# Kernel optimization log

Hardware: AMD Instinct MI355X
Metric: run time of the kernel (lower is better)

The kernel has to match this reference:

```python
import jax, jax.numpy as jnp
import numpy as np

S, D, H, G, DH = 2048, 4096, 32, 8, 128  # seq, d_in, heads, kv_groups, head_dim
GROUP = H // G


def rotate_half(x):
    x1, x2 = jnp.split(x, 2, axis=-1)
    return jnp.concatenate([-x2, x1], axis=-1)


def setup_inputs() -> dict:
    key = jax.random.key(0)
    ks = jax.random.split(key, 8)
    x = jax.random.normal(ks[0], (1, S, D), dtype=jnp.float32)
    # causal mask: True above the diagonal (positions to mask out)
    mask = jnp.triu(jnp.ones((S, S), dtype=bool), k=1)
    # standard RoPE tables
    inv_freq = 1.0 / (10000.0 ** (np.arange(0, DH, 2, dtype=np.float32) / DH))
    t = np.arange(S, dtype=np.float32)
    freqs = np.outer(t, inv_freq)                      # [S, DH/2]
    emb = np.concatenate([freqs, freqs], axis=-1)      # [S, DH]
    cos = jnp.asarray(np.cos(emb), dtype=jnp.float32)
    sin = jnp.asarray(np.sin(emb), dtype=jnp.float32)
    sc = 0.02
    Wq = jax.random.normal(ks[1], (D, H * DH), dtype=jnp.float32) * sc
    Wk = jax.random.normal(ks[2], (D, G * DH), dtype=jnp.float32) * sc
    Wv = jax.random.normal(ks[3], (D, G * DH), dtype=jnp.float32) * sc
    Wo = jax.random.normal(ks[4], (H * DH, D), dtype=jnp.float32) * sc
    return {"x": x, "mask": mask, "cos": cos, "sin": sin,
            "Wq": Wq, "Wk": Wk, "Wv": Wv, "Wo": Wo}


def reference(x, mask, cos, sin, Wq, Wk, Wv, Wo):
    xs = x[0]                                          # [S, D] (batch must be 1)
    q = (xs @ Wq).reshape(S, H, DH).transpose(1, 0, 2)   # [H, S, DH]
    k = (xs @ Wk).reshape(S, G, DH).transpose(1, 0, 2)   # [G, S, DH]
    v = (xs @ Wv).reshape(S, G, DH).transpose(1, 0, 2)   # [G, S, DH]
    # RoPE
    q = q * cos[None] + rotate_half(q) * sin[None]
    k = k * cos[None] + rotate_half(k) * sin[None]
    # GQA: repeat KV groups to match query heads
    k = jnp.repeat(k, GROUP, axis=0)                   # [H, S, DH]
    v = jnp.repeat(v, GROUP, axis=0)                   # [H, S, DH]
    scores = jnp.einsum('hsd,htd->hst', q, k)          # [H, S, S]
    scores = jnp.where(mask[None], -jnp.inf, scores)
    scores = scores / jnp.sqrt(jnp.float32(DH))
    w = jax.nn.softmax(scores, axis=-1)
    ctx = jnp.einsum('hst,htd->hsd', w, v)             # [H, S, DH]
    ctx = ctx.transpose(1, 0, 2).reshape(S, H * DH)
    out = ctx @ Wo                                     # [S, D]
    return out[None]                                   # [1, S, D]
```

## Files before the change

kernel.cpp:

```cpp
#include <hip/hip_runtime.h>
#include <hip/hip_bf16.h>
#include <cstdint>
#include <cstddef>

#define S 2048
#define D 4096
#define H 32
#define G 8
#define DH 128
#define HD (H*DH)
#define GD (G*DH)

typedef __bf16 bf16;
typedef __bf16 bf16x4 __attribute__((ext_vector_type(4)));
typedef __bf16 bf16x8 __attribute__((ext_vector_type(8)));
typedef float f32x4 __attribute__((ext_vector_type(4)));

__device__ __forceinline__ void gload16(const void* g, void* l) {
    __builtin_amdgcn_global_load_lds(
        (const __attribute__((address_space(1))) void*)g,
        (__attribute__((address_space(3))) void*)l, 16, 0, 0);
}

#define FENCE() asm volatile("" ::: "memory")
#define BARRIER() do { FENCE(); __builtin_amdgcn_s_barrier(); FENCE(); } while (0)
#define LGKM0()  do { asm volatile("s_waitcnt lgkmcnt(0)" ::: "memory"); \
                      __builtin_amdgcn_sched_barrier(0); } while (0)
#define VMCNT(n) asm volatile("s_waitcnt vmcnt(" #n ")" ::: "memory")

__global__ __launch_bounds__(256) void cast_f32_bf16(const float* __restrict__ in,
                                                     bf16* __restrict__ out, int n4)
{
    int i = blockIdx.x * 256 + threadIdx.x;
    if (i < n4) {
        float4 v = reinterpret_cast<const float4*>(in)[i];
        bf16x4 o = { (bf16)v.x, (bf16)v.y, (bf16)v.z, (bf16)v.w };
        reinterpret_cast<bf16x4*>(out)[i] = o;
    }
}

template<bool IN_F32>
__global__ __launch_bounds__(256) void transpose_to_bf16(
    const void* __restrict__ in, bf16* __restrict__ out, int R, int C)
{
    const int r0 = blockIdx.y * 64 + (threadIdx.x & 7) * 8;
    const int c0 = blockIdx.x * 256 + (threadIdx.x >> 3) * 8;
    bf16 m[8][8];
    #pragma unroll
    for (int j = 0; j < 8; ++j) {
        if constexpr (IN_F32) {
            const float* p = (const float*)in + (size_t)(r0 + j) * C + c0;
            float4 a = *reinterpret_cast<const float4*>(p);
            float4 b = *reinterpret_cast<const float4*>(p + 4);
            m[j][0] = (bf16)a.x; m[j][1] = (bf16)a.y; m[j][2] = (bf16)a.z; m[j][3] = (bf16)a.w;
            m[j][4] = (bf16)b.x; m[j][5] = (bf16)b.y; m[j][6] = (bf16)b.z; m[j][7] = (bf16)b.w;
        } else {
            const bf16* p = (const bf16*)in + (size_t)(r0 + j) * C + c0;
            bf16x8 v = *reinterpret_cast<const bf16x8*>(p);
            #pragma unroll
            for (int i = 0; i < 8; ++i) m[j][i] = v[i];
        }
    }
    #pragma unroll
    for (int i = 0; i < 8; ++i) {
        bf16x8 ov;
        #pragma unroll
        for (int j = 0; j < 8; ++j) ov[j] = m[j][i];
        *reinterpret_cast<bf16x8*>(out + (size_t)(c0 + i) * R + r0) = ov;
    }
}

__global__ __launch_bounds__(256) void rope_inplace(bf16* __restrict__ Y,
                                                    const float* __restrict__ cosT,
                                                    const float* __restrict__ sinT,
                                                    int ncols, int total, float scale)
{
    int idx = blockIdx.x * 256 + threadIdx.x;
    if (idx >= total) return;
    int pairs = ncols >> 1;
    int s = idx / pairs;
    int p = idx - s * pairs;
    int head = p >> 6;
    int d = p & 63;
    size_t base = (size_t)s * ncols + head * DH;
    float c  = cosT[s * DH + d];
    float sn = sinT[s * DH + d];
    float a = (float)Y[base + d];
    float b = (float)Y[base + d + 64];
    Y[base + d]      = (bf16)((a * c - b * sn) * scale);
    Y[base + d + 64] = (bf16)((b * c + a * sn) * scale);
}

__global__ __launch_bounds__(512) void gemm192(
    const bf16* __restrict__ A, const bf16* __restrict__ Bt,
    bf16* __restrict__ Qout, bf16* __restrict__ Kout, bf16* __restrict__ Vout, int K)
{
    extern __shared__ char smem[];
    const int tid = threadIdx.x, lane = tid & 63, wave = tid >> 6;
    const int wr = wave >> 2, wc = wave & 3;
    const int l15 = lane & 15, lhi = lane >> 4;
    const int r8 = lane >> 3, c8 = lane & 7;
    const int csw = ((c8 ^ r8) << 3);

    const int bid = blockIdx.x;
    const int swz = (bid & 7) * 32 + (bid >> 3);
    const int bm = (swz >> 5) * 256, bn = (swz & 31) * 192;
    const int NT = K >> 6;

    auto stA = [&](int buf, int u, int t) {
        gload16(A + (size_t)(bm + u * 64 + wave * 8 + r8) * K + (t << 6) + csw,
                smem + buf * 57344 + u * 8192 + wave * 1024);
    };
    auto stB = [&](int buf, int u, int t) {
        gload16(Bt + (size_t)(bn + u * 64 + wave * 8 + r8) * K + (t << 6) + csw,
                smem + buf * 57344 + 32768 + u * 8192 + wave * 1024);
    };
    auto rdA = [&](const char* Cb, int mh, int ks, bf16x8* af) {
        #pragma unroll
        for (int m = 0; m < 4; ++m) {
            int row = wr * 128 + mh * 64 + m * 16 + l15;
            int ch = (ks * 4 + lhi) ^ (l15 & 7);
            af[m] = *reinterpret_cast<const bf16x8*>(Cb + row * 128 + ch * 16);
        }
    };
    auto rdB = [&](const char* Cb, int ks, bf16x8* bfv) {
        #pragma unroll
        for (int n = 0; n < 3; ++n) {
            int row = wc * 48 + n * 16 + l15;
            int ch = (ks * 4 + lhi) ^ (l15 & 7);
            bfv[n] = *reinterpret_cast<const bf16x8*>(Cb + 32768 + row * 128 + ch * 16);
        }
    };

    f32x4 acc[8][3] = {};

    auto mm = [&](int mh, const bf16x8* af, const bf16x8* bfv) {
        LGKM0();
        __builtin_amdgcn_s_setprio(1);
        #pragma unroll
        for (int m = 0; m < 4; ++m)
            #pragma unroll
            for (int n = 0; n < 3; ++n)
                acc[mh * 4 + m][n] = __builtin_amdgcn_mfma_f32_16x16x32_bf16(
                    af[m], bfv[n], acc[mh * 4 + m][n], 0, 0, 0);
        __builtin_amdgcn_s_setprio(0);
    };

    stB(0, 0, 0); stB(0, 1, 0); stB(0, 2, 0);
    stA(0, 0, 0); stA(0, 2, 0); stA(0, 1, 0); stA(0, 3, 0);
    VMCNT(2);
    BARRIER();

    for (int t = 0; t < NT; ++t) {
        const char* Cb = smem + (t & 1) * 57344;
        const int nb = (t + 1) & 1;
        const int tn = (t + 1 < NT) ? t + 1 : t;
        bf16x8 a4[4], bk0[3], bk1[3];

        rdB(Cb, 0, bk0); rdA(Cb, 0, 0, a4);
        stB(nb, 0, tn); stB(nb, 1, tn);
        mm(0, a4, bk0);
        BARRIER();

        rdB(Cb, 1, bk1); rdA(Cb, 0, 1, a4);
        stB(nb, 2, tn); stA(nb, 0, tn);
        mm(0, a4, bk1);
        VMCNT(4);
        BARRIER();

        rdA(Cb, 1, 0, a4);
        stA(nb, 2, tn); stA(nb, 1, tn);
        mm(1, a4, bk0);
        BARRIER();

        rdA(Cb, 1, 1, a4);
        stA(nb, 3, tn);
        mm(1, a4, bk1);
        VMCNT(2);
        BARRIER();
    }

    #pragma unroll
    for (int m = 0; m < 8; ++m) {
        int r0 = bm + wr * 128 + m * 16 + lhi * 4;
        #pragma unroll
        for (int n = 0; n < 3; ++n) {
            int c = bn + wc * 48 + n * 16 + l15;
            #pragma unroll
            for (int j = 0; j < 4; ++j) {
                bf16 v = (bf16)acc[m][n][j];
                if (c < HD)            Qout[(size_t)(r0 + j) * HD + c] = v;
                else if (c < HD + GD)  Kout[(size_t)(r0 + j) * GD + (c - HD)] = v;
                else                   Vout[(size_t)(r0 + j) * GD + (c - HD - GD)] = v;
            }
        }
    }
}

__global__ __launch_bounds__(512) void gemm3b(
    const bf16* __restrict__ A, const bf16* __restrict__ Bt,
    float* __restrict__ C, int N, int K, int nbn)
{
    extern __shared__ char smem[];
    const int tid = threadIdx.x, lane = tid & 63, wave = tid >> 6;
    const int wr = wave >> 1, wc = wave & 1;
    const int l15 = lane & 15, lhi = lane >> 4;
    const int r8 = lane >> 3, c8 = lane & 7;
    const int csw = ((c8 ^ r8) << 3);

    const int nwg = gridDim.x, qq = nwg >> 3;
    const int swz = (blockIdx.x & 7) * qq + (blockIdx.x >> 3);
    const int bm = (swz / nbn) * 256, bn = (swz % nbn) * 128;
    const int NT = K >> 6;

    auto stageA = [&](int buf, int L, int t) {
        int row0 = L * 64 + wave * 8;
        gload16(A + (size_t)(bm + row0 + r8) * K + (t << 6) + csw,
                smem + buf * 49152 + row0 * 128);
    };
    auto stageB = [&](int buf, int L, int t) {
        int row0 = L * 64 + wave * 8;
        gload16(Bt + (size_t)(bn + row0 + r8) * K + (t << 6) + csw,
                smem + buf * 49152 + 32768 + row0 * 128);
    };
    auto rdA = [&](const char* Ab, int ks, bf16x8* af) {
        #pragma unroll
        for (int m = 0; m < 4; ++m) {
            int row = wr * 64 + m * 16 + l15;
            int ch = (ks * 4 + lhi) ^ (l15 & 7);
            af[m] = *reinterpret_cast<const bf16x8*>(Ab + row * 128 + ch * 16);
        }
    };
    auto rdB = [&](const char* Bb, int ks, bf16x8* bfv) {
        #pragma unroll
        for (int n = 0; n < 4; ++n) {
            int row = wc * 64 + n * 16 + l15;
            int ch = (ks * 4 + lhi) ^ (l15 & 7);
            bfv[n] = *reinterpret_cast<const bf16x8*>(Bb + row * 128 + ch * 16);
        }
    };

    f32x4 acc[4][4] = {};

    #pragma unroll
    for (int L = 0; L < 4; ++L) stageA(0, L, 0);
    stageB(0, 0, 0); stageB(0, 1, 0);
    #pragma unroll
    for (int L = 0; L < 4; ++L) stageA(1, L, 1);
    stageB(1, 0, 1); stageB(1, 1, 1);
    VMCNT(6);
    BARRIER();

    for (int t = 0; t < NT; ++t) {
        const char* Ab = smem + (t % 3) * 49152;
        const char* Bb = Ab + 32768;
        const int b2 = (t + 2) % 3;
        const int st = (t + 2 < NT) ? t + 2 : NT - 1;
        bf16x8 af[4], bk[4];

        rdB(Bb, 0, bk); rdA(Ab, 0, af);
        stageA(b2, 0, st); stageA(b2, 1, st);
        LGKM0();
        __builtin_amdgcn_s_setprio(1);
        #pragma unroll
        for (int m = 0; m < 4; ++m)
            #pragma unroll
            for (int n = 0; n < 4; ++n)
                acc[m][n] = __builtin_amdgcn_mfma_f32_16x16x32_bf16(af[m], bk[n], acc[m][n], 0, 0, 0);
        __builtin_amdgcn_s_setprio(0);

        rdB(Bb, 1, bk); rdA(Ab, 1, af);
        stageA(b2, 2, st); stageA(b2, 3, st);
        stageB(b2, 0, st); stageB(b2, 1, st);
        LGKM0();
        __builtin_amdgcn_s_setprio(1);
        #pragma unroll
        for (int m = 0; m < 4; ++m)
            #pragma unroll
            for (int n = 0; n < 4; ++n)
                acc[m][n] = __builtin_amdgcn_mfma_f32_16x16x32_bf16(af[m], bk[n], acc[m][n], 0, 0, 0);
        __builtin_amdgcn_s_setprio(0);

        VMCNT(6);
        BARRIER();
    }

    #pragma unroll
    for (int m = 0; m < 4; ++m) {
        int r0 = bm + wr * 64 + m * 16 + lhi * 4;
        #pragma unroll
        for (int n = 0; n < 4; ++n) {
            int c = bn + wc * 64 + n * 16 + l15;
            #pragma unroll
            for (int j = 0; j < 4; ++j)
                C[(size_t)(r0 + j) * N + c] = acc[m][n][j];
        }
    }
}

#define BM 128
#define BN 128
#define BK 32
#define LDSK 40

template<bool OUT_BF16>
__global__ __launch_bounds__(256) void gemm_aBf16(
    const bf16* __restrict__ A,
    const float* __restrict__ B0, const float* __restrict__ B1,
    void* __restrict__ C0, void* __restrict__ C1,
    int M, int N, int K)
{
    __shared__ alignas(16) bf16 Al[BM][LDSK];
    __shared__ alignas(16) bf16 Bt[BN][LDSK];

    const float* __restrict__ B = blockIdx.z ? B1 : B0;
    void* __restrict__ C = blockIdx.z ? C1 : C0;

    const int tid  = threadIdx.x;
    const int lane = tid & 63;
    const int wave = tid >> 6;
    const int wm = (wave >> 1) * 64;
    const int wn = (wave & 1) * 64;
    const int bm = blockIdx.y * BM;
    const int bn = blockIdx.x * BN;
    const int l15 = lane & 15;
    const int lhi = lane >> 4;

    f32x4 acc[4][4] = {};

    for (int k0 = 0; k0 < K; k0 += BK) {
        #pragma unroll
        for (int it = 0; it < 2; ++it) {
            int idx = it * 256 + tid;
            int row = idx >> 2;
            int ko  = idx & 3;
            bf16x8 v = *reinterpret_cast<const bf16x8*>(
                A + (size_t)(bm + row) * K + k0 + ko * 8);
            *reinterpret_cast<bf16x8*>(&Al[row][ko * 8]) = v;
        }
        {
            int n = tid & 127;
            int kbase = (tid >> 7) * 8;
            const float* bp = B + (size_t)k0 * N + bn + n;
            #pragma unroll
            for (int half = 0; half < 2; ++half) {
                bf16x8 v;
                #pragma unroll
                for (int j = 0; j < 8; ++j)
                    v[j] = (bf16)bp[(size_t)(half * 16 + kbase + j) * N];
                *reinterpret_cast<bf16x8*>(&Bt[n][half * 16 + kbase]) = v;
            }
        }
        __syncthreads();

        bf16x8 af[4], bfv[4];
        #pragma unroll
        for (int m = 0; m < 4; ++m)
            af[m] = *reinterpret_cast<const bf16x8*>(&Al[wm + m * 16 + l15][lhi * 8]);
        #pragma unroll
        for (int n = 0; n < 4; ++n)
            bfv[n] = *reinterpret_cast<const bf16x8*>(&Bt[wn + n * 16 + l15][lhi * 8]);
        #pragma unroll
        for (int m = 0; m < 4; ++m)
            #pragma unroll
            for (int n = 0; n < 4; ++n)
                acc[m][n] = __builtin_amdgcn_mfma_f32_16x16x32_bf16(
                    af[m], bfv[n], acc[m][n], 0, 0, 0);
        __syncthreads();
    }

    #pragma unroll
    for (int m = 0; m < 4; ++m) {
        int r0 = bm + wm + m * 16 + lhi * 4;
        #pragma unroll
        for (int n = 0; n < 4; ++n) {
            int c = bn + wn + n * 16 + l15;
            #pragma unroll
            for (int j = 0; j < 4; ++j) {
                if constexpr (OUT_BF16)
                    reinterpret_cast<bf16*>(C)[(size_t)(r0 + j) * N + c] = (bf16)acc[m][n][j];
                else
                    reinterpret_cast<float*>(C)[(size_t)(r0 + j) * N + c] = acc[m][n][j];
            }
        }
    }
}

#define QBLK 64
#define KVBLK 64
#define NQT (S/QBLK)

template<bool MASK>
__device__ __forceinline__ void attn_tile(
    int t0, int q0, int wave, int l15, int lhi,
    const bf16x8* qf, const char* Kl, const char* Vl, char* Plw,
    f32x4* o, float* m_i, float* l_i)
{
    f32x4 sc[4] = {};
    __builtin_amdgcn_s_setprio(1);
    #pragma unroll
    for (int n = 0; n < 4; ++n) {
        int row = n * 16 + l15;
        #pragma unroll
        for (int kk = 0; kk < 4; ++kk) {
            bf16x8 kf = *reinterpret_cast<const bf16x8*>(
                Kl + row * 256 + ((((kk * 4 + lhi)) ^ (l15 & 7)) << 4));
            sc[n] = __builtin_amdgcn_mfma_f32_16x16x32_bf16(qf[kk], kf, sc[n], 0, 0, 0);
        }
    }
    __builtin_amdgcn_s_setprio(0);

    float corr[4];
    #pragma unroll
    for (int j = 0; j < 4; ++j) {
        const int qr = q0 + wave * 16 + lhi * 4 + j;
        float vals[4];
        float mx = -1e30f;
        #pragma unroll
        for (int n = 0; n < 4; ++n) {
            float v = sc[n][j];
            if constexpr (MASK) {
                int t = t0 + n * 16 + l15;
                if (t > qr) v = -1e30f;
            }
            vals[n] = v;
            mx = fmaxf(mx, v);
        }
        #pragma unroll
        for (int ms = 1; ms < 16; ms <<= 1)
            mx = fmaxf(mx, __shfl_xor(mx, ms, 16));
        float mnew = fmaxf(m_i[j], mx);
        float cr = __expf(m_i[j] - mnew);
        float rsum = 0.f;
        #pragma unroll
        for (int n = 0; n < 4; ++n) {
            float p = __expf(vals[n] - mnew);
            rsum += p;
            int r = lhi * 4 + j;
            int off = ((r << 7) + ((n * 16 + l15) << 1)) ^ ((r & 7) << 4);
            *reinterpret_cast<bf16*>(Plw + off) = (bf16)p;
        }
        #pragma unroll
        for (int ms = 1; ms < 16; ms <<= 1)
            rsum += __shfl_xor(rsum, ms, 16);
        l_i[j] = l_i[j] * cr + rsum;
        m_i[j] = mnew;
        corr[j] = cr;
    }

    #pragma unroll
    for (int n = 0; n < 8; ++n)
        #pragma unroll
        for (int j = 0; j < 4; ++j)
            o[n][j] *= corr[j];

    __builtin_amdgcn_s_setprio(1);
    #pragma unroll
    for (int kk = 0; kk < 2; ++kk) {
        bf16x8 pf = *reinterpret_cast<const bf16x8*>(
            Plw + (l15 << 7) + ((((kk * 4 + lhi)) ^ (l15 & 7)) << 4));
        #pragma unroll
        for (int n = 0; n < 8; ++n) {
            int d = n * 16 + l15;
            bf16x8 vf = *reinterpret_cast<const bf16x8*>(
                Vl + (d << 7) + ((((kk * 4 + lhi)) ^ (d & 7)) << 4));
            o[n] = __builtin_amdgcn_mfma_f32_16x16x32_bf16(pf, vf, o[n], 0, 0, 0);
        }
    }
    __builtin_amdgcn_s_setprio(0);
}

__global__ __launch_bounds__(256) void flash_fwd3(
    const bf16* __restrict__ Q, const bf16* __restrict__ Kr,
    const bf16* __restrict__ VtG, bf16* __restrict__ ctx)
{
    extern __shared__ char fsm[];

    const int tid  = threadIdx.x;
    const int lane = tid & 63;
    const int wave = tid >> 6;
    const int l15 = lane & 15;
    const int lhi = lane >> 4;
    const int bid = blockIdx.x;
    const int qt = (NQT - 1) - (bid >> 5);
    const int h  = ((bid & 7) << 2) | ((bid >> 3) & 3);
    const int g  = h >> 2;
    const int q0 = qt * QBLK;
    char* Plw = fsm + 65536 + wave * 2048;

    bf16x8 qf[4];
    {
        const bf16* qp = Q + (size_t)(q0 + wave * 16 + l15) * HD + h * DH + lhi * 8;
        #pragma unroll
        for (int kk = 0; kk < 4; ++kk)
            qf[kk] = *reinterpret_cast<const bf16x8*>(qp + kk * 32);
    }

    f32x4 o[8] = {};
    float m_i[4] = { -1e30f, -1e30f, -1e30f, -1e30f };
    float l_i[4] = {};

    auto stage = [&](int t0, int buf) {
        char* Kl = fsm + buf * 32768;
        char* Vl = Kl + 16384;
        #pragma unroll
        for (int t = 0; t < 4; ++t) {
            int ch = wave * 256 + t * 64 + lane;
            {
                int row = ch >> 4, ci = ch & 15;
                gload16(Kr + (size_t)(t0 + row) * GD + g * DH + ((ci ^ (row & 7)) << 3),
                        Kl + (wave * 256 + t * 64) * 16);
            }
            {
                int d = ch >> 3, ci = ch & 7;
                gload16(VtG + (size_t)(g * DH + d) * S + t0 + ((ci ^ (d & 7)) << 3),
                        Vl + (wave * 256 + t * 64) * 16);
            }
        }
    };

    const int nt = qt + 1;
    stage(0, 0);
    VMCNT(0);
    BARRIER();

    for (int it = 0; it < nt; ++it) {
        if (it + 1 < nt) stage((it + 1) * KVBLK, (it + 1) & 1);
        const char* Kl = fsm + (it & 1) * 32768;
        const char* Vl = Kl + 16384;
        if (it == nt - 1)
            attn_tile<true>(it * KVBLK, q0, wave, l15, lhi, qf, Kl, Vl, Plw, o, m_i, l_i);
        else
            attn_tile<false>(it * KVBLK, q0, wave, l15, lhi, qf, Kl, Vl, Plw, o, m_i, l_i);
        VMCNT(0);
        BARRIER();
    }

    #pragma unroll
    for (int n = 0; n < 8; ++n) {
        int c = h * DH + n * 16 + l15;
        #pragma unroll
        for (int j = 0; j < 4; ++j) {
            int r = q0 + wave * 16 + lhi * 4 + j;
            ctx[(size_t)r * HD + c] = (bf16)(o[n][j] / l_i[j]);
        }
    }
}

extern "C" void kernel_launch(void* const* d_in, const int* in_sizes, int n_in,
                              void* d_out, int out_size, void* d_ws, size_t ws_size,
                              hipStream_t stream)
{
    const float* x    = (const float*)d_in[0];
    const float* cosT = (const float*)d_in[2];
    const float* sinT = (const float*)d_in[3];
    const float* Wq   = (const float*)d_in[4];
    const float* Wk   = (const float*)d_in[5];
    const float* Wv   = (const float*)d_in[6];
    const float* Wo   = (const float*)d_in[7];
    float* out = (float*)d_out;

    const size_t MB = (size_t)1 << 20;
    char* ws = (char*)d_ws;
    bf16* xb  = (bf16*)ws;
    bf16* ctx = (bf16*)(ws + 16 * MB);
    bf16* Qb  = (bf16*)d_out;
    bf16* Kb  = Qb + (size_t)S * HD;
    bf16* Vb  = Kb + (size_t)S * GD;
    bf16* VtG = Vb + (size_t)S * GD;

    const bool fast = ws_size >= 112 * MB;
    const float qscale = 0.08838834764831845f;

    hipFuncSetAttribute(reinterpret_cast<const void*>(&flash_fwd3),
                        hipFuncAttributeMaxDynamicSharedMemorySize, 73728);

    cast_f32_bf16<<<(S * D / 4 + 255) / 256, 256, 0, stream>>>(x, xb, S * D / 4);

    if (fast) {
        bf16* Wqkvt = (bf16*)(ws + 32 * MB);
        bf16* Wot   = (bf16*)(ws + 80 * MB);

        transpose_to_bf16<true><<<dim3(HD / 256, D / 64), 256, 0, stream>>>(Wq, Wqkvt, D, HD);
        transpose_to_bf16<true><<<dim3(GD / 256, D / 64), 256, 0, stream>>>(Wk, Wqkvt + (size_t)HD * D, D, GD);
        transpose_to_bf16<true><<<dim3(GD / 256, D / 64), 256, 0, stream>>>(Wv, Wqkvt + (size_t)(HD + GD) * D, D, GD);
        transpose_to_bf16<true><<<dim3(D / 256, HD / 64), 256, 0, stream>>>(Wo, Wot, HD, D);

        hipFuncSetAttribute(reinterpret_cast<const void*>(&gemm192),
                            hipFuncAttributeMaxDynamicSharedMemorySize, 114688);
        hipFuncSetAttribute(reinterpret_cast<const void*>(&gemm3b),
                            hipFuncAttributeMaxDynamicSharedMemorySize, 147456);

        gemm192<<<256, 512, 114688, stream>>>(xb, Wqkvt, Qb, Kb, Vb, D);

        rope_inplace<<<(S * HD / 2 + 255) / 256, 256, 0, stream>>>(Qb, cosT, sinT, HD, S * HD / 2, qscale);
        rope_inplace<<<(S * GD / 2 + 255) / 256, 256, 0, stream>>>(Kb, cosT, sinT, GD, S * GD / 2, 1.0f);

        transpose_to_bf16<false><<<dim3(GD / 256, S / 64), 256, 0, stream>>>(Vb, VtG, S, GD);

        flash_fwd3<<<NQT * H, 256, 73728, stream>>>(Qb, Kb, VtG, ctx);

        gemm3b<<<256, 512, 147456, stream>>>(ctx, Wot, out, D, HD, 32);
    } else {
        gemm_aBf16<true><<<dim3(HD / BN, S / BM, 1), 256, 0, stream>>>(
            xb, Wq, Wq, (void*)Qb, (void*)Qb, S, HD, D);
        gemm_aBf16<true><<<dim3(GD / BN, S / BM, 2), 256, 0, stream>>>(
            xb, Wk, Wv, (void*)Kb, (void*)Vb, S, GD, D);

        rope_inplace<<<(S * HD / 2 + 255) / 256, 256, 0, stream>>>(Qb, cosT, sinT, HD, S * HD / 2, qscale);
        rope_inplace<<<(S * GD / 2 + 255) / 256, 256, 0, stream>>>(Kb, cosT, sinT, GD, S * GD / 2, 1.0f);

        transpose_to_bf16<false><<<dim3(GD / 256, S / 64), 256, 0, stream>>>(Vb, VtG, S, GD);

        flash_fwd3<<<NQT * H, 256, 73728, stream>>>(Qb, Kb, VtG, ctx);

        gemm_aBf16<false><<<dim3(D / BN, S / BM, 1), 256, 0, stream>>>(
            ctx, Wo, Wo, (void*)out, (void*)out, S, D, HD);
    }

    (void)in_sizes; (void)n_in; (void)out_size; (void)ws_size;
}
```

Before: 365.4 us.

## Software-pipeline LDS reads in GEMMs and widen flash attention to 128-row Q tiles

Both projection GEMMs now prefetch the next k-slice's register fragments from LDS while MFMAs run on the current ones. Each issues a whole tile's global-to-LDS loads at once and uses partial lgkmcnt waits instead of draining to zero, which is meant to hide LDS latency behind matrix math. Flash attention moves to 512-thread blocks with 128-row query tiles and a larger shared-memory budget, so each K/V tile is reused by twice as many query rows. The costs are more register pressure, extra barriers per iteration, and fewer attention blocks. The launch_bounds occupancy hints and the changed masking logic may also affect correctness or occupancy.

```diff
diff --git a/kernel.cpp b/kernel.cpp
--- a/kernel.cpp
+++ b/kernel.cpp
@@ -24,9 +24,9 @@
 
 #define FENCE() asm volatile("" ::: "memory")
 #define BARRIER() do { FENCE(); __builtin_amdgcn_s_barrier(); FENCE(); } while (0)
-#define LGKM0()  do { asm volatile("s_waitcnt lgkmcnt(0)" ::: "memory"); \
-                      __builtin_amdgcn_sched_barrier(0); } while (0)
-#define VMCNT(n) asm volatile("s_waitcnt vmcnt(" #n ")" ::: "memory")
+#define VMCNT(n)  asm volatile("s_waitcnt vmcnt(" #n ")" ::: "memory")
+#define LGKMC(n)  do { asm volatile("s_waitcnt lgkmcnt(" #n ")" ::: "memory"); \
+                       __builtin_amdgcn_sched_barrier(0); } while (0)
 
 __global__ __launch_bounds__(256) void cast_f32_bf16(const float* __restrict__ in,
                                                      bf16* __restrict__ out, int n4)
@@ -91,7 +91,7 @@
     Y[base + d + 64] = (bf16)((b * c + a * sn) * scale);
 }
 
-__global__ __launch_bounds__(512) void gemm192(
+__global__ __launch_bounds__(512, 2) void gemm192(
     const bf16* __restrict__ A, const bf16* __restrict__ Bt,
     bf16* __restrict__ Qout, bf16* __restrict__ Kout, bf16* __restrict__ Vout, int K)
 {
@@ -107,13 +107,15 @@
     const int bm = (swz >> 5) * 256, bn = (swz & 31) * 192;
     const int NT = K >> 6;
 
-    auto stA = [&](int buf, int u, int t) {
-        gload16(A + (size_t)(bm + u * 64 + wave * 8 + r8) * K + (t << 6) + csw,
-                smem + buf * 57344 + u * 8192 + wave * 1024);
-    };
-    auto stB = [&](int buf, int u, int t) {
-        gload16(Bt + (size_t)(bn + u * 64 + wave * 8 + r8) * K + (t << 6) + csw,
-                smem + buf * 57344 + 32768 + u * 8192 + wave * 1024);
+    auto stageAll = [&](int buf, int t) {
+        #pragma unroll
+        for (int u = 0; u < 3; ++u)
+            gload16(Bt + (size_t)(bn + u * 64 + wave * 8 + r8) * K + (t << 6) + csw,
+                    smem + buf * 57344 + 32768 + u * 8192 + wave * 1024);
+        #pragma unroll
+        for (int u = 0; u < 4; ++u)
+            gload16(A + (size_t)(bm + u * 64 + wave * 8 + r8) * K + (t << 6) + csw,
+                    smem + buf * 57344 + u * 8192 + wave * 1024);
     };
     auto rdA = [&](const char* Cb, int mh, int ks, bf16x8* af) {
         #pragma unroll
@@ -133,9 +135,7 @@
     };
 
     f32x4 acc[8][3] = {};
-
-    auto mm = [&](int mh, const bf16x8* af, const bf16x8* bfv) {
-        LGKM0();
+    auto mmc = [&](int mh, const bf16x8* af, const bf16x8* bfv) {
         __builtin_amdgcn_s_setprio(1);
         #pragma unroll
         for (int m = 0; m < 4; ++m)
@@ -146,37 +146,43 @@
         __builtin_amdgcn_s_setprio(0);
     };
 
-    stB(0, 0, 0); stB(0, 1, 0); stB(0, 2, 0);
-    stA(0, 0, 0); stA(0, 2, 0); stA(0, 1, 0); stA(0, 3, 0);
-    VMCNT(2);
+    bf16x8 a_cur[4], a_nxt[4], bk0[3], bk1[3];
+
+    stageAll(0, 0);
+    VMCNT(0);
     BARRIER();
+    rdB(smem, 0, bk0);
+    rdA(smem, 0, 0, a_cur);
 
     for (int t = 0; t < NT; ++t) {
-        const char* Cb = smem + (t & 1) * 57344;
+        const char* cur = smem + (t & 1) * 57344;
+        const char* nxb = smem + ((t + 1) & 1) * 57344;
         const int nb = (t + 1) & 1;
         const int tn = (t + 1 < NT) ? t + 1 : t;
-        bf16x8 a4[4], bk0[3], bk1[3];
-
-        rdB(Cb, 0, bk0); rdA(Cb, 0, 0, a4);
-        stB(nb, 0, tn); stB(nb, 1, tn);
-        mm(0, a4, bk0);
-        BARRIER();
-
-        rdB(Cb, 1, bk1); rdA(Cb, 0, 1, a4);
-        stB(nb, 2, tn); stA(nb, 0, tn);
-        mm(0, a4, bk1);
-        VMCNT(4);
-        BARRIER();
-
-        rdA(Cb, 1, 0, a4);
-        stA(nb, 2, tn); stA(nb, 1, tn);
-        mm(1, a4, bk0);
-        BARRIER();
-
-        rdA(Cb, 1, 1, a4);
-        stA(nb, 3, tn);
-        mm(1, a4, bk1);
-        VMCNT(2);
+
+        rdA(cur, 0, 1, a_nxt);
+        rdB(cur, 1, bk1);
+        stageAll(nb, tn);
+        LGKMC(7);
+        mmc(0, a_cur, bk0);
+        BARRIER();
+
+        rdA(cur, 1, 0, a_cur);
+        LGKMC(4);
+        mmc(0, a_nxt, bk1);
+        BARRIER();
+
+        rdA(cur, 1, 1, a_nxt);
+        LGKMC(4);
+        mmc(1, a_cur, bk0);
+        BARRIER();
+
+        VMCNT(0);
+        BARRIER();
+        rdA(nxb, 0, 0, a_cur);
+        rdB(nxb, 0, bk0);
+        LGKMC(7);
+        mmc(1, a_nxt, bk1);
         BARRIER();
     }
 
@@ -197,7 +203,7 @@
     }
 }
 
-__global__ __launch_bounds__(512) void gemm3b(
+__global__ __launch_bounds__(512, 2) void gemm3b(
     const bf16* __restrict__ A, const bf16* __restrict__ Bt,
     float* __restrict__ C, int N, int K, int nbn)
 {
@@ -213,15 +219,15 @@
     const int bm = (swz / nbn) * 256, bn = (swz % nbn) * 128;
     const int NT = K >> 6;
 
-    auto stageA = [&](int buf, int L, int t) {
-        int row0 = L * 64 + wave * 8;
-        gload16(A + (size_t)(bm + row0 + r8) * K + (t << 6) + csw,
-                smem + buf * 49152 + row0 * 128);
-    };
-    auto stageB = [&](int buf, int L, int t) {
-        int row0 = L * 64 + wave * 8;
-        gload16(Bt + (size_t)(bn + row0 + r8) * K + (t << 6) + csw,
-                smem + buf * 49152 + 32768 + row0 * 128);
+    auto stageAll = [&](int buf, int t) {
+        #pragma unroll
+        for (int u = 0; u < 4; ++u)
+            gload16(A + (size_t)(bm + u * 64 + wave * 8 + r8) * K + (t << 6) + csw,
+                    smem + buf * 49152 + u * 8192 + wave * 1024);
+        #pragma unroll
+        for (int u = 0; u < 2; ++u)
+            gload16(Bt + (size_t)(bn + u * 64 + wave * 8 + r8) * K + (t << 6) + csw,
+                    smem + buf * 49152 + 32768 + u * 8192 + wave * 1024);
     };
     auto rdA = [&](const char* Ab, int ks, bf16x8* af) {
         #pragma unroll
@@ -231,57 +237,54 @@
             af[m] = *reinterpret_cast<const bf16x8*>(Ab + row * 128 + ch * 16);
         }
     };
-    auto rdB = [&](const char* Bb, int ks, bf16x8* bfv) {
+    auto rdB = [&](const char* Ab, int ks, bf16x8* bfv) {
         #pragma unroll
         for (int n = 0; n < 4; ++n) {
             int row = wc * 64 + n * 16 + l15;
             int ch = (ks * 4 + lhi) ^ (l15 & 7);
-            bfv[n] = *reinterpret_cast<const bf16x8*>(Bb + row * 128 + ch * 16);
+            bfv[n] = *reinterpret_cast<const bf16x8*>(Ab + 32768 + row * 128 + ch * 16);
         }
     };
 
     f32x4 acc[4][4] = {};
-
-    #pragma unroll
-    for (int L = 0; L < 4; ++L) stageA(0, L, 0);
-    stageB(0, 0, 0); stageB(0, 1, 0);
-    #pragma unroll
-    for (int L = 0; L < 4; ++L) stageA(1, L, 1);
-    stageB(1, 0, 1); stageB(1, 1, 1);
+    auto mmc = [&](const bf16x8* af, const bf16x8* bfv) {
+        __builtin_amdgcn_s_setprio(1);
+        #pragma unroll
+        for (int m = 0; m < 4; ++m)
+            #pragma unroll
+            for (int n = 0; n < 4; ++n)
+                acc[m][n] = __builtin_amdgcn_mfma_f32_16x16x32_bf16(af[m], bfv[n], acc[m][n], 0, 0, 0);
+        __builtin_amdgcn_s_setprio(0);
+    };
+
+    bf16x8 a_cur[4], b_cur[4], a_nxt[4], b_nxt[4];
+
+    stageAll(0, 0);
+    stageAll(1, (1 < NT) ? 1 : 0);
     VMCNT(6);
     BARRIER();
+    rdA(smem, 0, a_cur);
+    rdB(smem, 0, b_cur);
 
     for (int t = 0; t < NT; ++t) {
-        const char* Ab = smem + (t % 3) * 49152;
-        const char* Bb = Ab + 32768;
-        const int b2 = (t + 2) % 3;
+        const char* cur = smem + (t % 3) * 49152;
+        const char* nxb = smem + ((t + 1) % 3) * 49152;
+        const int sb = (t + 2) % 3;
         const int st = (t + 2 < NT) ? t + 2 : NT - 1;
-        bf16x8 af[4], bk[4];
-
-        rdB(Bb, 0, bk); rdA(Ab, 0, af);
-        stageA(b2, 0, st); stageA(b2, 1, st);
-        LGKM0();
-        __builtin_amdgcn_s_setprio(1);
-        #pragma unroll
-        for (int m = 0; m < 4; ++m)
-            #pragma unroll
-            for (int n = 0; n < 4; ++n)
-                acc[m][n] = __builtin_amdgcn_mfma_f32_16x16x32_bf16(af[m], bk[n], acc[m][n], 0, 0, 0);
-        __builtin_amdgcn_s_setprio(0);
-
-        rdB(Bb, 1, bk); rdA(Ab, 1, af);
-        stageA(b2, 2, st); stageA(b2, 3, st);
-        stageB(b2, 0, st); stageB(b2, 1, st);
-        LGKM0();
-        __builtin_amdgcn_s_setprio(1);
-        #pragma unroll
-        for (int m = 0; m < 4; ++m)
-            #pragma unroll
-            for (int n = 0; n < 4; ++n)
-                acc[m][n] = __builtin_amdgcn_mfma_f32_16x16x32_bf16(af[m], bk[n], acc[m][n], 0, 0, 0);
-        __builtin_amdgcn_s_setprio(0);
+
+        rdA(cur, 1, a_nxt);
+        rdB(cur, 1, b_nxt);
+        stageAll(sb, st);
+        LGKMC(8);
+        mmc(a_cur, b_cur);
+        BARRIER();
 
         VMCNT(6);
+        BARRIER();
+        rdA(nxb, 0, a_cur);
+        rdB(nxb, 0, b_cur);
+        LGKMC(8);
+        mmc(a_nxt, b_nxt);
         BARRIER();
     }
 
@@ -386,7 +389,7 @@
     }
 }
 
-#define QBLK 64
+#define QBLK 128
 #define KVBLK 64
 #define NQT (S/QBLK)
 
@@ -470,7 +473,7 @@
     __builtin_amdgcn_s_setprio(0);
 }
 
-__global__ __launch_bounds__(256) void flash_fwd3(
+__global__ __launch_bounds__(512, 4) void flash_fwd4(
     const bf16* __restrict__ Q, const bf16* __restrict__ Kr,
     const bf16* __restrict__ VtG, bf16* __restrict__ ctx)
 {
@@ -504,22 +507,22 @@
         char* Kl = fsm + buf * 32768;
         char* Vl = Kl + 16384;
         #pragma unroll
-        for (int t = 0; t < 4; ++t) {
-            int ch = wave * 256 + t * 64 + lane;
+        for (int t = 0; t < 2; ++t) {
+            int ch = t * 512 + tid;
             {
                 int row = ch >> 4, ci = ch & 15;
                 gload16(Kr + (size_t)(t0 + row) * GD + g * DH + ((ci ^ (row & 7)) << 3),
-                        Kl + (wave * 256 + t * 64) * 16);
+                        Kl + ch * 16);
             }
             {
                 int d = ch >> 3, ci = ch & 7;
                 gload16(VtG + (size_t)(g * DH + d) * S + t0 + ((ci ^ (d & 7)) << 3),
-                        Vl + (wave * 256 + t * 64) * 16);
+                        Vl + ch * 16);
             }
         }
     };
 
-    const int nt = qt + 1;
+    const int nt = 2 * qt + 2;
     stage(0, 0);
     VMCNT(0);
     BARRIER();
@@ -528,7 +531,7 @@
         if (it + 1 < nt) stage((it + 1) * KVBLK, (it + 1) & 1);
         const char* Kl = fsm + (it & 1) * 32768;
         const char* Vl = Kl + 16384;
-        if (it == nt - 1)
+        if (it >= nt - 2)
             attn_tile<true>(it * KVBLK, q0, wave, l15, lhi, qf, Kl, Vl, Plw, o, m_i, l_i);
         else
             attn_tile<false>(it * KVBLK, q0, wave, l15, lhi, qf, Kl, Vl, Plw, o, m_i, l_i);
@@ -572,8 +575,8 @@
     const bool fast = ws_size >= 112 * MB;
     const float qscale = 0.08838834764831845f;
 
-    hipFuncSetAttribute(reinterpret_cast<const void*>(&flash_fwd3),
-                        hipFuncAttributeMaxDynamicSharedMemorySize, 73728);
+    hipFuncSetAttribute(reinterpret_cast<const void*>(&flash_fwd4),
+                        hipFuncAttributeMaxDynamicSharedMemorySize, 81920);
 
     cast_f32_bf16<<<(S * D / 4 + 255) / 256, 256, 0, stream>>>(x, xb, S * D / 4);
 
@@ -598,7 +601,7 @@
 
         transpose_to_bf16<false><<<dim3(GD / 256, S / 64), 256, 0, stream>>>(Vb, VtG, S, GD);
 
-        flash_fwd3<<<NQT * H, 256, 73728, stream>>>(Qb, Kb, VtG, ctx);
+        flash_fwd4<<<NQT * H, 512, 81920, stream>>>(Qb, Kb, VtG, ctx);
 
         gemm3b<<<256, 512, 147456, stream>>>(ctx, Wot, out, D, HD, 32);
     } else {
@@ -612,7 +615,7 @@
 
         transpose_to_bf16<false><<<dim3(GD / 256, S / 64), 256, 0, stream>>>(Vb, VtG, S, GD);
 
-        flash_fwd3<<<NQT * H, 256, 73728, stream>>>(Qb, Kb, VtG, ctx);
+        flash_fwd4<<<NQT * H, 512, 81920, stream>>>(Qb, Kb, VtG, ctx);
 
         gemm_aBf16<false><<<dim3(D / BN, S / BM, 1), 256, 0, stream>>>(
             ctx, Wo, Wo, (void*)out, (void*)out, S, D, HD);
```

After: 413.4 us. +13.1%, slower.
